# Kernel tuning notes

Hardware: AMD Instinct MI355X
Metric: run time of the kernel (lower is better)

## Reference

```python
import jax, jax.numpy as jnp
import numpy as np

TEMPERATURE = 1.0
NEG_BIG = -1.0e9


def _gumbel_softmax_hard(key, logits, temperature):
    # torch: rand_like().clamp(min=1e-10); -log(-log(u))
    u = jax.random.uniform(key, logits.shape, dtype=logits.dtype, minval=1e-10, maxval=1.0)
    g = -jnp.log(-jnp.log(u))
    y_soft = jax.nn.softmax((logits + g) / temperature, axis=-1)
    idx = jnp.argmax(y_soft, axis=-1)
    y_hard = jax.nn.one_hot(idx, logits.shape[-1], dtype=logits.dtype)
    # straight-through estimator
    return y_hard - jax.lax.stop_gradient(y_soft) + y_soft


def _eval_library(X, W1, b1, W2, b2):
    # X: (B, in_cols); W1: (M, in_cols, H); b1: (M, H); W2: (M, H); b2: (M,)
    h = jnp.tanh(jnp.einsum('bi,mih->mbh', X, W1) + b1[:, None, :])  # (M, B, H)
    return jnp.einsum('mbh,mh->bm', h, W2) + b2  # (B, M)


def setup_inputs() -> dict:
    key = jax.random.key(0)
    ks = jax.random.split(key, 8)
    B, S, M, H, IC, K = 32768, 2, 64, 128, 2, 2
    return {
        'X': jax.random.normal(ks[0], (B, IC), jnp.float32),
        'W1': jax.random.normal(ks[1], (M, IC, H), jnp.float32) * 0.3,
        'b1': jax.random.normal(ks[2], (M, H), jnp.float32) * 0.1,
        'W2': jax.random.normal(ks[3], (M, H), jnp.float32) * 0.3,
        'b2': jax.random.normal(ks[4], (M,), jnp.float32) * 0.1,
        'routers': jax.random.normal(ks[5], (S, M), jnp.float32),
        'coefficients': jax.random.normal(ks[6], (S, K, M), jnp.float32),
        'complexity_prior': jnp.zeros((M,), jnp.float32),
    }


def reference(X, W1, b1, W2, b2, routers, coefficients, complexity_prior):
    batch = X.shape[0]
    state_dim, k, n_mlps = coefficients.shape
    mlp_out = _eval_library(X, W1, b1, W2, b2)  # (B, M)

    gkey = jax.random.key(42)
    dXdt_pred, all_gates = [], []
    for d in range(state_dim):
        base_logits = jnp.broadcast_to((routers[d] + complexity_prior)[None, :], (batch, n_mlps))
        mask = jnp.zeros((batch, n_mlps), X.dtype)
        dxdt_d = jnp.zeros((batch,), X.dtype)
        slot_gates = []
        for j in range(k):
            kj = jax.random.fold_in(gkey, d * k + j)
            gate_j = _gumbel_softmax_hard(kj, base_logits + mask, TEMPERATURE)
            slot_gates.append(gate_j)
            mask = mask + NEG_BIG * jax.lax.stop_gradient(gate_j)
            dxdt_d = dxdt_d + jnp.sum(gate_j * coefficients[d, j][None, :] * mlp_out, axis=1)
        all_gates.append(jnp.stack(slot_gates, axis=0))  # (k, B, M)
        dXdt_pred.append(dxdt_d)
    return jnp.stack(dXdt_pred, axis=1), jnp.stack(all_gates, axis=0)
```

## Files before the change

### kernel.cpp

```cpp
#include <hip/hip_runtime.h>
#include <stdint.h>

#define BATCH 32768
#define NM 64

struct Keys { uint32_t k[8]; };

__host__ __device__ inline void threefry2x32(uint32_t k0, uint32_t k1,
                                             uint32_t x0, uint32_t x1,
                                             uint32_t* o0, uint32_t* o1) {
  uint32_t k2 = k0 ^ k1 ^ 0x1BD11BDAu;
  x0 += k0; x1 += k1;
#define TF_RND(r) { x0 += x1; x1 = (x1 << (r)) | (x1 >> (32 - (r))); x1 ^= x0; }
  TF_RND(13) TF_RND(15) TF_RND(26) TF_RND(6)
  x0 += k1; x1 += k2 + 1u;
  TF_RND(17) TF_RND(29) TF_RND(16) TF_RND(24)
  x0 += k2; x1 += k0 + 2u;
  TF_RND(13) TF_RND(15) TF_RND(26) TF_RND(6)
  x0 += k0; x1 += k1 + 3u;
  TF_RND(17) TF_RND(29) TF_RND(16) TF_RND(24)
  x0 += k1; x1 += k2 + 4u;
  TF_RND(13) TF_RND(15) TF_RND(26) TF_RND(6)
  x0 += k2; x1 += k0 + 5u;
#undef TF_RND
  *o0 = x0; *o1 = x1;
}

__device__ inline float gumbel_g(uint32_t bits) {
  float f = __uint_as_float((bits >> 9) | 0x3F800000u) - 1.0f;
  float u = fmaxf(1e-10f, f + 1e-10f);
  return -logf(-logf(u));
}

__device__ inline float tanh_fast(float x) {
  float e = __expf(2.0f * x);
#if __has_builtin(__builtin_amdgcn_rcpf)
  float r = __builtin_amdgcn_rcpf(e + 1.0f);
#else
  float r = 1.0f / (e + 1.0f);
#endif
  return fmaf(-2.0f, r, 1.0f);
}

__global__ __launch_bounds__(256) void k_fused(Keys keys,
    const float* __restrict__ X,   const float* __restrict__ W1,
    const float* __restrict__ b1v, const float* __restrict__ W2,
    const float* __restrict__ b2v, const float* __restrict__ routers,
    const float* __restrict__ coef, const float* __restrict__ cp,
    float* __restrict__ out0, float4* __restrict__ gates) {
  const int t = threadIdx.x;
  const int wv = t >> 6, lane = t & 63;
  const int b0w = blockIdx.x * 16 + wv * 4;

  const int g = lane >> 2, sub = lane & 3;
  const int dj = g & 3, bl = g >> 2;
  const uint32_t k0 = keys.k[dj * 2 + 0], k1 = keys.k[dj * 2 + 1];
  const uint32_t ibase = (uint32_t)(b0w + bl) * NM + (uint32_t)sub * 16;

  const float4* rq = (const float4*)(routers + (dj >> 1) * NM + sub * 16);
  const float4* cq = (const float4*)(cp + sub * 16);
  const float4 r0 = rq[0], r1 = rq[1], r2 = rq[2], r3 = rq[3];
  const float4 c0 = cq[0], c1 = cq[1], c2 = cq[2], c3 = cq[3];
  const float bvr[16] = {r0.x + c0.x, r0.y + c0.y, r0.z + c0.z, r0.w + c0.w,
                         r1.x + c1.x, r1.y + c1.y, r1.z + c1.z, r1.w + c1.w,
                         r2.x + c2.x, r2.y + c2.y, r2.z + c2.z, r2.w + c2.w,
                         r3.x + c3.x, r3.y + c3.y, r3.z + c3.z, r3.w + c3.w};

  float best = -1e30f, second = -1e30f;
  int bi = 0, si = 0;
#pragma unroll
  for (int mm = 0; mm < 16; ++mm) {
    uint32_t o0, o1;
    threefry2x32(k0, k1, 0u, ibase + (uint32_t)mm, &o0, &o1);
    float z = bvr[mm] + gumbel_g(o0 ^ o1);
    int m = sub * 16 + mm;
    if (z > best)        { second = best; si = bi; best = z; bi = m; }
    else if (z > second) { second = z; si = m; }
  }
#pragma unroll
  for (int dlt = 1; dlt <= 2; dlt <<= 1) {
    float ob = __shfl_xor(best, dlt);  int obi = __shfl_xor(bi, dlt);
    float os = __shfl_xor(second, dlt); int osi = __shfl_xor(si, dlt);
    bool selfWins = (best > ob) || (best == ob && bi < obi);
    if (selfWins) {
      if (ob > second || (ob == second && obi < si)) { second = ob; si = obi; }
    } else {
      if (best > os || (best == os && bi < osi)) { second = best; si = bi; }
      else { second = os; si = osi; }
      best = ob; bi = obi;
    }
  }
  const int w0p = __shfl_xor(bi, 4);
  const int w = ((g & 1) == 0) ? bi : ((bi == w0p) ? si : bi);

  {
    const int gb = lane >> 4, q = lane & 15;
    const int m0 = q * 4;
#pragma unroll
    for (int it = 0; it < 4; ++it) {
      const int gw = __shfl(w, (gb * 4 + it) * 4);
      float4 v;
      v.x = (m0 + 0 == gw) ? 1.0f : 0.0f;
      v.y = (m0 + 1 == gw) ? 1.0f : 0.0f;
      v.z = (m0 + 2 == gw) ? 1.0f : 0.0f;
      v.w = (m0 + 3 == gw) ? 1.0f : 0.0f;
      gates[((size_t)it * BATCH + b0w + gb) * 16 + q] = v;
    }
  }

  const int grp = lane >> 4, sl = lane & 15;
  const char* W1b = (const char*)W1;
  const char* B1b = (const char*)b1v;
  const char* W2b = (const char*)W2;
#pragma unroll
  for (int i = 0; i < 4; ++i) {
    const int rw = __shfl(w, (i * 4 + grp) * 4);
    const int brow = b0w + i;
    const float xa = X[brow * 2 + 0], xb = X[brow * 2 + 1];
    const int off  = (rw << 10) + (sl << 5);
    const int off2 = (rw << 9)  + (sl << 5);
    const float4 a0a = *(const float4*)(W1b + off);
    const float4 a0b = *(const float4*)(W1b + off + 16);
    const float4 a1a = *(const float4*)(W1b + off + 512);
    const float4 a1b = *(const float4*)(W1b + off + 528);
    const float4 b1a = *(const float4*)(B1b + off2);
    const float4 b1b = *(const float4*)(B1b + off2 + 16);
    const float4 w2a = *(const float4*)(W2b + off2);
    const float4 w2b = *(const float4*)(W2b + off2 + 16);
    float h0 = fmaf(xb, a1a.x, fmaf(xa, a0a.x, b1a.x));
    float h1 = fmaf(xb, a1a.y, fmaf(xa, a0a.y, b1a.y));
    float h2 = fmaf(xb, a1a.z, fmaf(xa, a0a.z, b1a.z));
    float h3 = fmaf(xb, a1a.w, fmaf(xa, a0a.w, b1a.w));
    float h4 = fmaf(xb, a1b.x, fmaf(xa, a0b.x, b1b.x));
    float h5 = fmaf(xb, a1b.y, fmaf(xa, a0b.y, b1b.y));
    float h6 = fmaf(xb, a1b.z, fmaf(xa, a0b.z, b1b.z));
    float h7 = fmaf(xb, a1b.w, fmaf(xa, a0b.w, b1b.w));
    float s = tanh_fast(h0) * w2a.x;
    s = fmaf(tanh_fast(h1), w2a.y, s);
    s = fmaf(tanh_fast(h2), w2a.z, s);
    s = fmaf(tanh_fast(h3), w2a.w, s);
    s = fmaf(tanh_fast(h4), w2b.x, s);
    s = fmaf(tanh_fast(h5), w2b.y, s);
    s = fmaf(tanh_fast(h6), w2b.z, s);
    s = fmaf(tanh_fast(h7), w2b.w, s);
#pragma unroll
    for (int sft = 1; sft < 16; sft <<= 1) s += __shfl_xor(s, sft);
    const float val = coef[grp * NM + rw] * (s + b2v[rw]);
    const float pv = __shfl_xor(val, 16);
    if ((grp & 1) == 0 && sl == 0)
      out0[brow * 2 + (grp >> 1)] = val + pv;
  }
}

extern "C" void kernel_launch(void* const* d_in, const int* in_sizes, int n_in,
                              void* d_out, int out_size, void* d_ws, size_t ws_size,
                              hipStream_t stream) {
  const float* X       = (const float*)d_in[0];
  const float* W1      = (const float*)d_in[1];
  const float* b1v     = (const float*)d_in[2];
  const float* W2      = (const float*)d_in[3];
  const float* b2v     = (const float*)d_in[4];
  const float* routers = (const float*)d_in[5];
  const float* coef    = (const float*)d_in[6];
  const float* cp      = (const float*)d_in[7];
  float* out0  = (float*)d_out;
  float* gates = out0 + BATCH * 2;

  Keys keys;
  for (uint32_t dj = 0; dj < 4; ++dj) {
    uint32_t o0, o1;
    threefry2x32(0u, 42u, 0u, dj, &o0, &o1);
    keys.k[dj * 2 + 0] = o0;
    keys.k[dj * 2 + 1] = o1;
  }

  k_fused<<<dim3(BATCH / 16), dim3(256), 0, stream>>>(
      keys, X, W1, b1v, W2, b2v, routers, coef, cp, out0, (float4*)gates);
}
```

Before: 35.35 us.

## Remap work so each wave handles one batch row across all slots

Each wave now processes a single batch row: 16 lanes per (state, slot) pair, each lane generating 4 Gumbel samples instead of 16, with a wider shuffle reduction for argmax. Gate writes and the MLP evaluation no longer need cross-lane broadcast loops over 4 rows, and the grid grows 4x. This trades per-lane serial threefry work for more threads and more blocks, which adds parallelism but also raises launch and per-block overhead.

```diff
diff --git a/kernel.cpp b/kernel.cpp
--- a/kernel.cpp
+++ b/kernel.cpp
@@ -50,35 +50,29 @@
     float* __restrict__ out0, float4* __restrict__ gates) {
   const int t = threadIdx.x;
   const int wv = t >> 6, lane = t & 63;
-  const int b0w = blockIdx.x * 16 + wv * 4;
+  const int brow = blockIdx.x * 4 + wv;
 
-  const int g = lane >> 2, sub = lane & 3;
-  const int dj = g & 3, bl = g >> 2;
+  const int dj = lane >> 4, s = lane & 15;
   const uint32_t k0 = keys.k[dj * 2 + 0], k1 = keys.k[dj * 2 + 1];
-  const uint32_t ibase = (uint32_t)(b0w + bl) * NM + (uint32_t)sub * 16;
+  const uint32_t ibase = (uint32_t)brow * NM + (uint32_t)s * 4;
 
-  const float4* rq = (const float4*)(routers + (dj >> 1) * NM + sub * 16);
-  const float4* cq = (const float4*)(cp + sub * 16);
-  const float4 r0 = rq[0], r1 = rq[1], r2 = rq[2], r3 = rq[3];
-  const float4 c0 = cq[0], c1 = cq[1], c2 = cq[2], c3 = cq[3];
-  const float bvr[16] = {r0.x + c0.x, r0.y + c0.y, r0.z + c0.z, r0.w + c0.w,
-                         r1.x + c1.x, r1.y + c1.y, r1.z + c1.z, r1.w + c1.w,
-                         r2.x + c2.x, r2.y + c2.y, r2.z + c2.z, r2.w + c2.w,
-                         r3.x + c3.x, r3.y + c3.y, r3.z + c3.z, r3.w + c3.w};
+  const float4 rr = *(const float4*)(routers + (dj >> 1) * NM + s * 4);
+  const float4 cc = *(const float4*)(cp + s * 4);
+  const float bvr[4] = {rr.x + cc.x, rr.y + cc.y, rr.z + cc.z, rr.w + cc.w};
 
   float best = -1e30f, second = -1e30f;
   int bi = 0, si = 0;
 #pragma unroll
-  for (int mm = 0; mm < 16; ++mm) {
+  for (int k = 0; k < 4; ++k) {
     uint32_t o0, o1;
-    threefry2x32(k0, k1, 0u, ibase + (uint32_t)mm, &o0, &o1);
-    float z = bvr[mm] + gumbel_g(o0 ^ o1);
-    int m = sub * 16 + mm;
+    threefry2x32(k0, k1, 0u, ibase + (uint32_t)k, &o0, &o1);
+    float z = bvr[k] + gumbel_g(o0 ^ o1);
+    int m = s * 4 + k;
     if (z > best)        { second = best; si = bi; best = z; bi = m; }
     else if (z > second) { second = z; si = m; }
   }
 #pragma unroll
-  for (int dlt = 1; dlt <= 2; dlt <<= 1) {
+  for (int dlt = 1; dlt <= 8; dlt <<= 1) {
     float ob = __shfl_xor(best, dlt);  int obi = __shfl_xor(bi, dlt);
     float os = __shfl_xor(second, dlt); int osi = __shfl_xor(si, dlt);
     bool selfWins = (best > ob) || (best == ob && bi < obi);
@@ -90,66 +84,55 @@
       best = ob; bi = obi;
     }
   }
-  const int w0p = __shfl_xor(bi, 4);
-  const int w = ((g & 1) == 0) ? bi : ((bi == w0p) ? si : bi);
+  const int w0p = __shfl_xor(bi, 16);
+  const int w = ((dj & 1) == 0) ? bi : ((bi == w0p) ? si : bi);
 
   {
-    const int gb = lane >> 4, q = lane & 15;
-    const int m0 = q * 4;
-#pragma unroll
-    for (int it = 0; it < 4; ++it) {
-      const int gw = __shfl(w, (gb * 4 + it) * 4);
-      float4 v;
-      v.x = (m0 + 0 == gw) ? 1.0f : 0.0f;
-      v.y = (m0 + 1 == gw) ? 1.0f : 0.0f;
-      v.z = (m0 + 2 == gw) ? 1.0f : 0.0f;
-      v.w = (m0 + 3 == gw) ? 1.0f : 0.0f;
-      gates[((size_t)it * BATCH + b0w + gb) * 16 + q] = v;
-    }
+    const int m0 = s * 4;
+    float4 v;
+    v.x = (m0 + 0 == w) ? 1.0f : 0.0f;
+    v.y = (m0 + 1 == w) ? 1.0f : 0.0f;
+    v.z = (m0 + 2 == w) ? 1.0f : 0.0f;
+    v.w = (m0 + 3 == w) ? 1.0f : 0.0f;
+    gates[((size_t)dj * BATCH + brow) * 16 + s] = v;
   }
 
-  const int grp = lane >> 4, sl = lane & 15;
+  const float xa = X[brow * 2 + 0], xb = X[brow * 2 + 1];
   const char* W1b = (const char*)W1;
   const char* B1b = (const char*)b1v;
   const char* W2b = (const char*)W2;
+  const int off  = (w << 10) + (s << 5);
+  const int off2 = (w << 9)  + (s << 5);
+  const float4 a0a = *(const float4*)(W1b + off);
+  const float4 a0b = *(const float4*)(W1b + off + 16);
+  const float4 a1a = *(const float4*)(W1b + off + 512);
+  const float4 a1b = *(const float4*)(W1b + off + 528);
+  const float4 b1a = *(const float4*)(B1b + off2);
+  const float4 b1b = *(const float4*)(B1b + off2 + 16);
+  const float4 w2a = *(const float4*)(W2b + off2);
+  const float4 w2b = *(const float4*)(W2b + off2 + 16);
+  float h0 = fmaf(xb, a1a.x, fmaf(xa, a0a.x, b1a.x));
+  float h1 = fmaf(xb, a1a.y, fmaf(xa, a0a.y, b1a.y));
+  float h2 = fmaf(xb, a1a.z, fmaf(xa, a0a.z, b1a.z));
+  float h3 = fmaf(xb, a1a.w, fmaf(xa, a0a.w, b1a.w));
+  float h4 = fmaf(xb, a1b.x, fmaf(xa, a0b.x, b1b.x));
+  float h5 = fmaf(xb, a1b.y, fmaf(xa, a0b.y, b1b.y));
+  float h6 = fmaf(xb, a1b.z, fmaf(xa, a0b.z, b1b.z));
+  float h7 = fmaf(xb, a1b.w, fmaf(xa, a0b.w, b1b.w));
+  float sum = tanh_fast(h0) * w2a.x;
+  sum = fmaf(tanh_fast(h1), w2a.y, sum);
+  sum = fmaf(tanh_fast(h2), w2a.z, sum);
+  sum = fmaf(tanh_fast(h3), w2a.w, sum);
+  sum = fmaf(tanh_fast(h4), w2b.x, sum);
+  sum = fmaf(tanh_fast(h5), w2b.y, sum);
+  sum = fmaf(tanh_fast(h6), w2b.z, sum);
+  sum = fmaf(tanh_fast(h7), w2b.w, sum);
 #pragma unroll
-  for (int i = 0; i < 4; ++i) {
-    const int rw = __shfl(w, (i * 4 + grp) * 4);
-    const int brow = b0w + i;
-    const float xa = X[brow * 2 + 0], xb = X[brow * 2 + 1];
-    const int off  = (rw << 10) + (sl << 5);
-    const int off2 = (rw << 9)  + (sl << 5);
-    const float4 a0a = *(const float4*)(W1b + off);
-    const float4 a0b = *(const float4*)(W1b + off + 16);
-    const float4 a1a = *(const float4*)(W1b + off + 512);
-    const float4 a1b = *(const float4*)(W1b + off + 528);
-    const float4 b1a = *(const float4*)(B1b + off2);
-    const float4 b1b = *(const float4*)(B1b + off2 + 16);
-    const float4 w2a = *(const float4*)(W2b + off2);
-    const float4 w2b = *(const float4*)(W2b + off2 + 16);
-    float h0 = fmaf(xb, a1a.x, fmaf(xa, a0a.x, b1a.x));
-    float h1 = fmaf(xb, a1a.y, fmaf(xa, a0a.y, b1a.y));
-    float h2 = fmaf(xb, a1a.z, fmaf(xa, a0a.z, b1a.z));
-    float h3 = fmaf(xb, a1a.w, fmaf(xa, a0a.w, b1a.w));
-    float h4 = fmaf(xb, a1b.x, fmaf(xa, a0b.x, b1b.x));
-    float h5 = fmaf(xb, a1b.y, fmaf(xa, a0b.y, b1b.y));
-    float h6 = fmaf(xb, a1b.z, fmaf(xa, a0b.z, b1b.z));
-    float h7 = fmaf(xb, a1b.w, fmaf(xa, a0b.w, b1b.w));
-    float s = tanh_fast(h0) * w2a.x;
-    s = fmaf(tanh_fast(h1), w2a.y, s);
-    s = fmaf(tanh_fast(h2), w2a.z, s);
-    s = fmaf(tanh_fast(h3), w2a.w, s);
-    s = fmaf(tanh_fast(h4), w2b.x, s);
-    s = fmaf(tanh_fast(h5), w2b.y, s);
-    s = fmaf(tanh_fast(h6), w2b.z, s);
-    s = fmaf(tanh_fast(h7), w2b.w, s);
-#pragma unroll
-    for (int sft = 1; sft < 16; sft <<= 1) s += __shfl_xor(s, sft);
-    const float val = coef[grp * NM + rw] * (s + b2v[rw]);
-    const float pv = __shfl_xor(val, 16);
-    if ((grp & 1) == 0 && sl == 0)
-      out0[brow * 2 + (grp >> 1)] = val + pv;
-  }
+  for (int sft = 1; sft <= 8; sft <<= 1) sum += __shfl_xor(sum, sft);
+  const float val = coef[dj * NM + w] * (sum + b2v[w]);
+  const float pv = __shfl_xor(val, 16);
+  if ((dj & 1) == 0 && s == 0)
+    out0[brow * 2 + (dj >> 1)] = val + pv;
 }
 
 extern "C" void kernel_launch(void* const* d_in, const int* in_sizes, int n_in,
@@ -174,6 +157,6 @@
     keys.k[dj * 2 + 1] = o1;
   }
 
-  k_fused<<<dim3(BATCH / 16), dim3(256), 0, stream>>>(
+  k_fused<<<dim3(BATCH / 4), dim3(256), 0, stream>>>(
       keys, X, W1, b1v, W2, b2v, routers, coef, cp, out0, (float4*)gates);
 }
```

After: 37.43 us. 1.06x slower.
